# Kernel tuning notes

Hardware: AMD Instinct MI355X
Metric: run time of the kernel (lower is better)

The kernel has to match this reference:

```python
import jax, jax.numpy as jnp
import numpy as np

B, N = 256, 16384


def setup_inputs() -> dict:
    key = jax.random.key(0)
    k1, k2, k3 = jax.random.split(key, 3)
    pred_coords = jax.random.normal(k1, (B, N, 3), dtype=jnp.float32)
    true_coords = jax.random.normal(k2, (B, N, 3), dtype=jnp.float32)
    weights = jax.random.uniform(k3, (B, N), dtype=jnp.float32)
    mask = jnp.ones((B, N), dtype=bool)
    return {"pred_coords": pred_coords, "true_coords": true_coords,
            "weights": weights, "mask": mask}


def reference(pred_coords, true_coords, weights, mask):
    # Mask out invalid atoms (Algorithm 28, weighted Kabsch alignment)
    pred = jnp.where(mask[..., None], pred_coords, 0.0)
    true = jnp.where(mask[..., None], true_coords, 0.0)
    w = jnp.where(mask, weights, 0.0)[..., None]            # [b, n, 1]

    wsum = w.sum(axis=1, keepdims=True)                     # [b, 1, 1]
    pred_centroid = (pred * w).sum(axis=1, keepdims=True) / wsum
    true_centroid = (true * w).sum(axis=1, keepdims=True) / wsum

    pred_c = pred - pred_centroid                           # [b, n, 3]
    true_c = true - true_centroid                           # [b, n, 3]

    # weighted covariance: [b, 3, 3]
    cov = jnp.einsum('bni,bnj->bij', true_c * w, pred_c)

    # torch.svd returns V (not V^T); jnp returns Vh = V^T. rot = U @ V^T = U @ Vh
    U, _, Vh = jnp.linalg.svd(cov)
    rot = jnp.einsum('bij,bjk->bik', U, Vh)

    # reflection fix: flip last column of V (= last row of Vh) where det < 0
    det = jnp.linalg.det(rot)                               # [b]
    flip = jnp.where(det < 0, -1.0, 1.0)                    # [b]
    Vh_fixed = Vh.at[:, -1, :].multiply(flip[:, None])
    rot = jnp.einsum('bij,bjk->bik', U, Vh_fixed)

    aligned = jnp.einsum('bni,bij->bnj', pred_c, rot) + true_centroid
    # original module calls .detach_() on the output
    return jax.lax.stop_gradient(aligned)
```

## Files before the change

kernel.cpp:

```cpp
#include <hip/hip_runtime.h>
#include <stdint.h>
#include <math.h>

constexpr int BATCH  = 256;
constexpr int NATOM  = 16384;
constexpr int TPB    = 256;
constexpr int APT    = 4;
constexpr int NQ     = 16;

constexpr int C1     = 4;
constexpr int ITERS  = 4;
constexpr int ABLK1  = NATOM / C1;

constexpr int C3     = 16;

typedef float f32x4 __attribute__((ext_vector_type(4)));
typedef int   i32x4 __attribute__((ext_vector_type(4)));

__global__ __launch_bounds__(TPB) void wra_partials(
    const float* __restrict__ pred, const float* __restrict__ tru,
    const float* __restrict__ wgt, const int* __restrict__ mask,
    float* __restrict__ partials)
{
    const int blk = blockIdx.x;
    const int b   = blk >> 2;
    const int s   = blk & 3;
    const int tid = threadIdx.x;

    float acc[NQ];
    #pragma unroll
    for (int k = 0; k < NQ; ++k) acc[k] = 0.f;

    #pragma unroll 2
    for (int it = 0; it < ITERS; ++it) {
        const long base = (long)b * NATOM + (long)s * ABLK1
                        + (long)it * (TPB * APT) + (long)tid * APT;

        const f32x4* p4 = reinterpret_cast<const f32x4*>(pred + base * 3);
        const f32x4* t4 = reinterpret_cast<const f32x4*>(tru  + base * 3);
        f32x4 pA = p4[0], pB = p4[1], pC = p4[2];
        f32x4 tA = __builtin_nontemporal_load(t4 + 0);
        f32x4 tB = __builtin_nontemporal_load(t4 + 1);
        f32x4 tC = __builtin_nontemporal_load(t4 + 2);
        f32x4 wv = __builtin_nontemporal_load(
                       reinterpret_cast<const f32x4*>(wgt + base));
        i32x4 mv = *reinterpret_cast<const i32x4*>(mask + base);

        float P[12] = {pA.x,pA.y,pA.z,pA.w, pB.x,pB.y,pB.z,pB.w, pC.x,pC.y,pC.z,pC.w};
        float T[12] = {tA.x,tA.y,tA.z,tA.w, tB.x,tB.y,tB.z,tB.w, tC.x,tC.y,tC.z,tC.w};
        float W[4]  = {mv.x ? wv.x : 0.f, mv.y ? wv.y : 0.f,
                       mv.z ? wv.z : 0.f, mv.w ? wv.w : 0.f};

        #pragma unroll
        for (int k = 0; k < APT; ++k) {
            float w  = W[k];
            float px = P[3*k], py = P[3*k+1], pz = P[3*k+2];
            float tx = T[3*k], ty = T[3*k+1], tz = T[3*k+2];
            float wtx = w * tx, wty = w * ty, wtz = w * tz;
            acc[0]  += w;
            acc[1]  += w * px;  acc[2]  += w * py;  acc[3]  += w * pz;
            acc[4]  += wtx;     acc[5]  += wty;     acc[6]  += wtz;
            acc[7]  += wtx*px;  acc[8]  += wtx*py;  acc[9]  += wtx*pz;
            acc[10] += wty*px;  acc[11] += wty*py;  acc[12] += wty*pz;
            acc[13] += wtz*px;  acc[14] += wtz*py;  acc[15] += wtz*pz;
        }
    }

    #pragma unroll
    for (int off = 32; off > 0; off >>= 1) {
        #pragma unroll
        for (int k = 0; k < NQ; ++k)
            acc[k] += __shfl_down(acc[k], off, 64);
    }
    __shared__ float red[4][NQ];
    const int wave = tid >> 6, lane = tid & 63;
    if (lane == 0) {
        #pragma unroll
        for (int k = 0; k < NQ; ++k) red[wave][k] = acc[k];
    }
    __syncthreads();
    if (tid < NQ)
        partials[blk * NQ + tid] =
            red[0][tid] + red[1][tid] + red[2][tid] + red[3][tid];
}

__device__ inline void jrot(double M[3][3], double V[3][3], int p, int q) {
    double mpq = M[p][q];
    if (fabs(mpq) < 1e-300) return;
    double theta = (M[q][q] - M[p][p]) / (2.0 * mpq);
    double t = copysign(1.0, theta) / (fabs(theta) + sqrt(theta * theta + 1.0));
    double c = 1.0 / sqrt(t * t + 1.0);
    double s = t * c;
    int r = 3 - p - q;
    double mpp = M[p][p], mqq = M[q][q], mrp = M[r][p], mrq = M[r][q];
    M[p][p] = mpp - t * mpq;
    M[q][q] = mqq + t * mpq;
    M[p][q] = M[q][p] = 0.0;
    double nrp = c * mrp - s * mrq;
    double nrq = s * mrp + c * mrq;
    M[r][p] = M[p][r] = nrp;
    M[r][q] = M[q][r] = nrq;
    #pragma unroll
    for (int i = 0; i < 3; ++i) {
        double vip = V[i][p], viq = V[i][q];
        V[i][p] = c * vip - s * viq;
        V[i][q] = s * vip + c * viq;
    }
}

__global__ __launch_bounds__(64) void wra_solve(
    const float* __restrict__ partials, float* __restrict__ consts)
{
    const int b = blockIdx.x, tid = threadIdx.x;
    __shared__ double q[NQ];
    if (tid < NQ) {
        double sum = 0.0;
        for (int s = 0; s < C1; ++s)
            sum += (double)partials[(b * C1 + s) * NQ + tid];
        q[tid] = sum;
    }
    __syncthreads();
    if (tid != 0) return;

    double wsum = q[0];
    double pc[3], tc[3];
    for (int j = 0; j < 3; ++j) { pc[j] = q[1+j] / wsum; tc[j] = q[4+j] / wsum; }

    double C[3][3];
    for (int i = 0; i < 3; ++i)
        for (int j = 0; j < 3; ++j)
            C[i][j] = q[7 + 3*i + j] - wsum * tc[i] * pc[j];

    double M[3][3];
    for (int i = 0; i < 3; ++i)
        for (int j = 0; j < 3; ++j)
            M[i][j] = C[0][i]*C[0][j] + C[1][i]*C[1][j] + C[2][i]*C[2][j];
    double V[3][3] = {{1,0,0},{0,1,0},{0,0,1}};
    for (int sweep = 0; sweep < 12; ++sweep) {
        double off = M[0][1]*M[0][1] + M[0][2]*M[0][2] + M[1][2]*M[1][2];
        double diag = M[0][0] + M[1][1] + M[2][2];
        if (off <= 1e-28 * diag * diag) break;
        jrot(M, V, 0, 1);
        jrot(M, V, 0, 2);
        jrot(M, V, 1, 2);
    }
    double lam[3] = {M[0][0], M[1][1], M[2][2]};
    int i0 = 0, i1 = 1, i2 = 2, tmp;
    if (lam[i0] < lam[i1]) { tmp = i0; i0 = i1; i1 = tmp; }
    if (lam[i0] < lam[i2]) { tmp = i0; i0 = i2; i2 = tmp; }
    if (lam[i1] < lam[i2]) { tmp = i1; i1 = i2; i2 = tmp; }
    double v0[3] = {V[0][i0], V[1][i0], V[2][i0]};
    double v1[3] = {V[0][i1], V[1][i1], V[2][i1]};
    double v2[3] = {V[0][i2], V[1][i2], V[2][i2]};

    double u0[3], u1[3];
    for (int i = 0; i < 3; ++i) {
        u0[i] = C[i][0]*v0[0] + C[i][1]*v0[1] + C[i][2]*v0[2];
        u1[i] = C[i][0]*v1[0] + C[i][1]*v1[1] + C[i][2]*v1[2];
    }
    double n0 = sqrt(u0[0]*u0[0] + u0[1]*u0[1] + u0[2]*u0[2]);
    for (int i = 0; i < 3; ++i) u0[i] /= n0;
    double d01 = u1[0]*u0[0] + u1[1]*u0[1] + u1[2]*u0[2];
    for (int i = 0; i < 3; ++i) u1[i] -= d01 * u0[i];
    double n1 = sqrt(u1[0]*u1[0] + u1[1]*u1[1] + u1[2]*u1[2]);
    for (int i = 0; i < 3; ++i) u1[i] /= n1;

    double detV = v0[0]*(v1[1]*v2[2] - v1[2]*v2[1])
                - v0[1]*(v1[0]*v2[2] - v1[2]*v2[0])
                + v0[2]*(v1[0]*v2[1] - v1[1]*v2[0]);
    double sV = (detV >= 0.0) ? 1.0 : -1.0;
    double u2[3] = { sV * (u0[1]*u1[2] - u0[2]*u1[1]),
                     sV * (u0[2]*u1[0] - u0[0]*u1[2]),
                     sV * (u0[0]*u1[1] - u0[1]*u1[0]) };

    float* out = consts + b * 15;
    for (int i = 0; i < 3; ++i)
        for (int j = 0; j < 3; ++j)
            out[3*i + j] = (float)(u0[i]*v0[j] + u1[i]*v1[j] + u2[i]*v2[j]);
    for (int j = 0; j < 3; ++j) { out[9 + j] = (float)pc[j]; out[12 + j] = (float)tc[j]; }
}

__global__ __launch_bounds__(TPB) void wra_apply(
    const float* __restrict__ pred, const int* __restrict__ mask,
    const float* __restrict__ consts, float* __restrict__ out)
{
    const int blk = blockIdx.x;
    const int b   = blk >> 4;
    const int s   = blk & 15;
    const int tid = threadIdx.x;

    __shared__ float c[15];
    if (tid < 15) c[tid] = consts[b * 15 + tid];
    __syncthreads();

    const long base = (long)b * NATOM + (long)s * (TPB * APT) + (long)tid * APT;
    const f32x4* p4 = reinterpret_cast<const f32x4*>(pred + base * 3);
    f32x4 pA = p4[0], pB = p4[1], pC = p4[2];
    i32x4 mv = *reinterpret_cast<const i32x4*>(mask + base);

    float P[12] = {pA.x,pA.y,pA.z,pA.w, pB.x,pB.y,pB.z,pB.w, pC.x,pC.y,pC.z,pC.w};
    int Mk[4] = {mv.x, mv.y, mv.z, mv.w};
    float O[12];

    #pragma unroll
    for (int k = 0; k < APT; ++k) {
        float px = (Mk[k] ? P[3*k]   : 0.f) - c[9];
        float py = (Mk[k] ? P[3*k+1] : 0.f) - c[10];
        float pz = (Mk[k] ? P[3*k+2] : 0.f) - c[11];
        O[3*k]   = px * c[0] + py * c[3] + pz * c[6] + c[12];
        O[3*k+1] = px * c[1] + py * c[4] + pz * c[7] + c[13];
        O[3*k+2] = px * c[2] + py * c[5] + pz * c[8] + c[14];
    }
    f32x4* o4 = reinterpret_cast<f32x4*>(out + base * 3);
    f32x4 o0 = {O[0], O[1], O[2],  O[3]};
    f32x4 o1 = {O[4], O[5], O[6],  O[7]};
    f32x4 o2 = {O[8], O[9], O[10], O[11]};
    __builtin_nontemporal_store(o0, o4 + 0);
    __builtin_nontemporal_store(o1, o4 + 1);
    __builtin_nontemporal_store(o2, o4 + 2);
}

extern "C" void kernel_launch(void* const* d_in, const int* in_sizes, int n_in,
                              void* d_out, int out_size, void* d_ws, size_t ws_size,
                              hipStream_t stream) {
    const float* pred = (const float*)d_in[0];
    const float* tru  = (const float*)d_in[1];
    const float* wgt  = (const float*)d_in[2];
    const int*   mask = (const int*)d_in[3];
    float* out = (float*)d_out;

    float* partials = (float*)d_ws;
    float* consts   = partials + BATCH * C1 * NQ;

    hipLaunchKernelGGL(wra_partials, dim3(BATCH * C1), dim3(TPB), 0, stream,
                       pred, tru, wgt, mask, partials);
    hipLaunchKernelGGL(wra_solve, dim3(BATCH), dim3(64), 0, stream,
                       partials, consts);
    hipLaunchKernelGGL(wra_apply, dim3(BATCH * C3), dim3(TPB), 0, stream,
                       pred, mask, consts, out);
}
```

Before: 192.8 us.

## Fuse partial reduction, SVD solve and apply into one kernel with flag sync

Merges the three kernels into a single kernel. The last block per batch, detected by an atomic counter, solves the 3x3 alignment, and all four blocks spin-wait on a per-batch flag before applying the rotation to their own atoms. Because each block re-reads the pred chunk it just streamed, that read can hit cache, and two launch boundaries disappear. The cost is an extra memset launch and a cross-block spin-wait: if not all 1024 blocks are co-resident, this relies on scheduling and a bounded timeout, which could produce wrong output if it expires.

```diff
diff --git a/kernel.cpp b/kernel.cpp
--- a/kernel.cpp
+++ b/kernel.cpp
@@ -2,86 +2,40 @@
 #include <stdint.h>
 #include <math.h>
 
-constexpr int BATCH  = 256;
-constexpr int NATOM  = 16384;
-constexpr int TPB    = 256;
-constexpr int APT    = 4;
-constexpr int NQ     = 16;
-
-constexpr int C1     = 4;
-constexpr int ITERS  = 4;
-constexpr int ABLK1  = NATOM / C1;
-
-constexpr int C3     = 16;
+constexpr int BATCH = 256;
+constexpr int NATOM = 16384;
+constexpr int TPB   = 256;
+constexpr int NQ    = 16;
+constexpr int C     = 4;
+constexpr int ABLK  = NATOM / C;
+constexpr int GRAN  = 4;
+
 
 typedef float f32x4 __attribute__((ext_vector_type(4)));
 typedef int   i32x4 __attribute__((ext_vector_type(4)));
 
-__global__ __launch_bounds__(TPB) void wra_partials(
-    const float* __restrict__ pred, const float* __restrict__ tru,
-    const float* __restrict__ wgt, const int* __restrict__ mask,
-    float* __restrict__ partials)
+__device__ __forceinline__ void accum4(
+    const f32x4 p0, const f32x4 p1, const f32x4 p2,
+    const f32x4 t0, const f32x4 t1, const f32x4 t2,
+    const f32x4 wv, const i32x4 mv, float* acc)
 {
-    const int blk = blockIdx.x;
-    const int b   = blk >> 2;
-    const int s   = blk & 3;
-    const int tid = threadIdx.x;
-
-    float acc[NQ];
-    #pragma unroll
-    for (int k = 0; k < NQ; ++k) acc[k] = 0.f;
-
-    #pragma unroll 2
-    for (int it = 0; it < ITERS; ++it) {
-        const long base = (long)b * NATOM + (long)s * ABLK1
-                        + (long)it * (TPB * APT) + (long)tid * APT;
-
-        const f32x4* p4 = reinterpret_cast<const f32x4*>(pred + base * 3);
-        const f32x4* t4 = reinterpret_cast<const f32x4*>(tru  + base * 3);
-        f32x4 pA = p4[0], pB = p4[1], pC = p4[2];
-        f32x4 tA = __builtin_nontemporal_load(t4 + 0);
-        f32x4 tB = __builtin_nontemporal_load(t4 + 1);
-        f32x4 tC = __builtin_nontemporal_load(t4 + 2);
-        f32x4 wv = __builtin_nontemporal_load(
-                       reinterpret_cast<const f32x4*>(wgt + base));
-        i32x4 mv = *reinterpret_cast<const i32x4*>(mask + base);
-
-        float P[12] = {pA.x,pA.y,pA.z,pA.w, pB.x,pB.y,pB.z,pB.w, pC.x,pC.y,pC.z,pC.w};
-        float T[12] = {tA.x,tA.y,tA.z,tA.w, tB.x,tB.y,tB.z,tB.w, tC.x,tC.y,tC.z,tC.w};
-        float W[4]  = {mv.x ? wv.x : 0.f, mv.y ? wv.y : 0.f,
-                       mv.z ? wv.z : 0.f, mv.w ? wv.w : 0.f};
-
-        #pragma unroll
-        for (int k = 0; k < APT; ++k) {
-            float w  = W[k];
-            float px = P[3*k], py = P[3*k+1], pz = P[3*k+2];
-            float tx = T[3*k], ty = T[3*k+1], tz = T[3*k+2];
-            float wtx = w * tx, wty = w * ty, wtz = w * tz;
-            acc[0]  += w;
-            acc[1]  += w * px;  acc[2]  += w * py;  acc[3]  += w * pz;
-            acc[4]  += wtx;     acc[5]  += wty;     acc[6]  += wtz;
-            acc[7]  += wtx*px;  acc[8]  += wtx*py;  acc[9]  += wtx*pz;
-            acc[10] += wty*px;  acc[11] += wty*py;  acc[12] += wty*pz;
-            acc[13] += wtz*px;  acc[14] += wtz*py;  acc[15] += wtz*pz;
-        }
-    }
-
-    #pragma unroll
-    for (int off = 32; off > 0; off >>= 1) {
-        #pragma unroll
-        for (int k = 0; k < NQ; ++k)
-            acc[k] += __shfl_down(acc[k], off, 64);
-    }
-    __shared__ float red[4][NQ];
-    const int wave = tid >> 6, lane = tid & 63;
-    if (lane == 0) {
-        #pragma unroll
-        for (int k = 0; k < NQ; ++k) red[wave][k] = acc[k];
-    }
-    __syncthreads();
-    if (tid < NQ)
-        partials[blk * NQ + tid] =
-            red[0][tid] + red[1][tid] + red[2][tid] + red[3][tid];
+    const float pf[12] = {p0.x,p0.y,p0.z,p0.w, p1.x,p1.y,p1.z,p1.w, p2.x,p2.y,p2.z,p2.w};
+    const float tf[12] = {t0.x,t0.y,t0.z,t0.w, t1.x,t1.y,t1.z,t1.w, t2.x,t2.y,t2.z,t2.w};
+    const float wf[4]  = {wv.x, wv.y, wv.z, wv.w};
+    const int   mf[4]  = {mv.x, mv.y, mv.z, mv.w};
+    #pragma unroll
+    for (int k = 0; k < 4; ++k) {
+        const float w  = (mf[k] != 0) ? wf[k] : 0.f;
+        const float px = pf[3*k], py = pf[3*k+1], pz = pf[3*k+2];
+        const float tx = tf[3*k], ty = tf[3*k+1], tz = tf[3*k+2];
+        const float wtx = w * tx, wty = w * ty, wtz = w * tz;
+        acc[0]  += w;
+        acc[1]  += w * px;  acc[2]  += w * py;  acc[3]  += w * pz;
+        acc[4]  += wtx;     acc[5]  += wty;     acc[6]  += wtz;
+        acc[7]  += wtx*px;  acc[8]  += wtx*py;  acc[9]  += wtx*pz;
+        acc[10] += wty*px;  acc[11] += wty*py;  acc[12] += wty*pz;
+        acc[13] += wtz*px;  acc[14] += wtz*py;  acc[15] += wtz*pz;
+    }
 }
 
 __device__ inline void jrot(double M[3][3], double V[3][3], int p, int q) {
@@ -108,116 +62,193 @@
     }
 }
 
-__global__ __launch_bounds__(64) void wra_solve(
-    const float* __restrict__ partials, float* __restrict__ consts)
-{
-    const int b = blockIdx.x, tid = threadIdx.x;
-    __shared__ double q[NQ];
-    if (tid < NQ) {
-        double sum = 0.0;
-        for (int s = 0; s < C1; ++s)
-            sum += (double)partials[(b * C1 + s) * NQ + tid];
-        q[tid] = sum;
-    }
-    __syncthreads();
-    if (tid != 0) return;
-
-    double wsum = q[0];
-    double pc[3], tc[3];
-    for (int j = 0; j < 3; ++j) { pc[j] = q[1+j] / wsum; tc[j] = q[4+j] / wsum; }
-
-    double C[3][3];
-    for (int i = 0; i < 3; ++i)
-        for (int j = 0; j < 3; ++j)
-            C[i][j] = q[7 + 3*i + j] - wsum * tc[i] * pc[j];
-
-    double M[3][3];
-    for (int i = 0; i < 3; ++i)
-        for (int j = 0; j < 3; ++j)
-            M[i][j] = C[0][i]*C[0][j] + C[1][i]*C[1][j] + C[2][i]*C[2][j];
-    double V[3][3] = {{1,0,0},{0,1,0},{0,0,1}};
-    for (int sweep = 0; sweep < 12; ++sweep) {
-        double off = M[0][1]*M[0][1] + M[0][2]*M[0][2] + M[1][2]*M[1][2];
-        double diag = M[0][0] + M[1][1] + M[2][2];
-        if (off <= 1e-28 * diag * diag) break;
-        jrot(M, V, 0, 1);
-        jrot(M, V, 0, 2);
-        jrot(M, V, 1, 2);
-    }
-    double lam[3] = {M[0][0], M[1][1], M[2][2]};
-    int i0 = 0, i1 = 1, i2 = 2, tmp;
-    if (lam[i0] < lam[i1]) { tmp = i0; i0 = i1; i1 = tmp; }
-    if (lam[i0] < lam[i2]) { tmp = i0; i0 = i2; i2 = tmp; }
-    if (lam[i1] < lam[i2]) { tmp = i1; i1 = i2; i2 = tmp; }
-    double v0[3] = {V[0][i0], V[1][i0], V[2][i0]};
-    double v1[3] = {V[0][i1], V[1][i1], V[2][i1]};
-    double v2[3] = {V[0][i2], V[1][i2], V[2][i2]};
-
-    double u0[3], u1[3];
-    for (int i = 0; i < 3; ++i) {
-        u0[i] = C[i][0]*v0[0] + C[i][1]*v0[1] + C[i][2]*v0[2];
-        u1[i] = C[i][0]*v1[0] + C[i][1]*v1[1] + C[i][2]*v1[2];
-    }
-    double n0 = sqrt(u0[0]*u0[0] + u0[1]*u0[1] + u0[2]*u0[2]);
-    for (int i = 0; i < 3; ++i) u0[i] /= n0;
-    double d01 = u1[0]*u0[0] + u1[1]*u0[1] + u1[2]*u0[2];
-    for (int i = 0; i < 3; ++i) u1[i] -= d01 * u0[i];
-    double n1 = sqrt(u1[0]*u1[0] + u1[1]*u1[1] + u1[2]*u1[2]);
-    for (int i = 0; i < 3; ++i) u1[i] /= n1;
-
-    double detV = v0[0]*(v1[1]*v2[2] - v1[2]*v2[1])
-                - v0[1]*(v1[0]*v2[2] - v1[2]*v2[0])
-                + v0[2]*(v1[0]*v2[1] - v1[1]*v2[0]);
-    double sV = (detV >= 0.0) ? 1.0 : -1.0;
-    double u2[3] = { sV * (u0[1]*u1[2] - u0[2]*u1[1]),
-                     sV * (u0[2]*u1[0] - u0[0]*u1[2]),
-                     sV * (u0[0]*u1[1] - u0[1]*u1[0]) };
-
-    float* out = consts + b * 15;
-    for (int i = 0; i < 3; ++i)
-        for (int j = 0; j < 3; ++j)
-            out[3*i + j] = (float)(u0[i]*v0[j] + u1[i]*v1[j] + u2[i]*v2[j]);
-    for (int j = 0; j < 3; ++j) { out[9 + j] = (float)pc[j]; out[12 + j] = (float)tc[j]; }
-}
-
-__global__ __launch_bounds__(TPB) void wra_apply(
-    const float* __restrict__ pred, const int* __restrict__ mask,
-    const float* __restrict__ consts, float* __restrict__ out)
+#define LOADG(Sfx, g) do {                                                   \
+    const long base_ = base0 + (long)(g) * (TPB * 4);                        \
+    const f32x4* p4_ = reinterpret_cast<const f32x4*>(pred + base_ * 3);     \
+    const f32x4* t4_ = reinterpret_cast<const f32x4*>(tru  + base_ * 3);     \
+    p##Sfx##0 = p4_[0]; p##Sfx##1 = p4_[1]; p##Sfx##2 = p4_[2];              \
+    t##Sfx##0 = t4_[0]; t##Sfx##1 = t4_[1]; t##Sfx##2 = t4_[2];              \
+    w##Sfx = *reinterpret_cast<const f32x4*>(wgt + base_);                   \
+    m##Sfx = *reinterpret_cast<const i32x4*>(mask + base_);                  \
+} while (0)
+
+__global__ __launch_bounds__(TPB, 4) void wra_fused(
+    const float* __restrict__ pred, const float* __restrict__ tru,
+    const float* __restrict__ wgt, const int* __restrict__ mask,
+    int* cnt, int* flag, float* partials, float* consts,
+    float* __restrict__ out)
 {
     const int blk = blockIdx.x;
-    const int b   = blk >> 4;
-    const int s   = blk & 15;
+    const int b   = blk >> 2;
+    const int s   = blk & 3;
     const int tid = threadIdx.x;
-
-    __shared__ float c[15];
-    if (tid < 15) c[tid] = consts[b * 15 + tid];
-    __syncthreads();
-
-    const long base = (long)b * NATOM + (long)s * (TPB * APT) + (long)tid * APT;
-    const f32x4* p4 = reinterpret_cast<const f32x4*>(pred + base * 3);
-    f32x4 pA = p4[0], pB = p4[1], pC = p4[2];
-    i32x4 mv = *reinterpret_cast<const i32x4*>(mask + base);
-
-    float P[12] = {pA.x,pA.y,pA.z,pA.w, pB.x,pB.y,pB.z,pB.w, pC.x,pC.y,pC.z,pC.w};
-    int Mk[4] = {mv.x, mv.y, mv.z, mv.w};
-    float O[12];
-
-    #pragma unroll
-    for (int k = 0; k < APT; ++k) {
-        float px = (Mk[k] ? P[3*k]   : 0.f) - c[9];
-        float py = (Mk[k] ? P[3*k+1] : 0.f) - c[10];
-        float pz = (Mk[k] ? P[3*k+2] : 0.f) - c[11];
-        O[3*k]   = px * c[0] + py * c[3] + pz * c[6] + c[12];
-        O[3*k+1] = px * c[1] + py * c[4] + pz * c[7] + c[13];
-        O[3*k+2] = px * c[2] + py * c[5] + pz * c[8] + c[14];
-    }
-    f32x4* o4 = reinterpret_cast<f32x4*>(out + base * 3);
-    f32x4 o0 = {O[0], O[1], O[2],  O[3]};
-    f32x4 o1 = {O[4], O[5], O[6],  O[7]};
-    f32x4 o2 = {O[8], O[9], O[10], O[11]};
-    __builtin_nontemporal_store(o0, o4 + 0);
-    __builtin_nontemporal_store(o1, o4 + 1);
-    __builtin_nontemporal_store(o2, o4 + 2);
+    const long base0 = (long)b * NATOM + (long)s * ABLK + (long)tid * 4;
+
+    float acc[NQ];
+    #pragma unroll
+    for (int k = 0; k < NQ; ++k) acc[k] = 0.f;
+
+    f32x4 pA0, pA1, pA2, tA0, tA1, tA2, wA;
+    f32x4 pB0, pB1, pB2, tB0, tB1, tB2, wB;
+    i32x4 mA, mB;
+
+    LOADG(A, 0);
+    LOADG(B, 1);
+    accum4(pA0, pA1, pA2, tA0, tA1, tA2, wA, mA, acc);
+    LOADG(A, 2);
+    accum4(pB0, pB1, pB2, tB0, tB1, tB2, wB, mB, acc);
+    LOADG(B, 3);
+    accum4(pA0, pA1, pA2, tA0, tA1, tA2, wA, mA, acc);
+    accum4(pB0, pB1, pB2, tB0, tB1, tB2, wB, mB, acc);
+
+    #pragma unroll
+    for (int off = 32; off >= 4; off >>= 1) {
+        #pragma unroll
+        for (int k = 0; k < NQ; ++k)
+            acc[k] += __shfl_down(acc[k], off, 64);
+    }
+    __shared__ float red[16][NQ + 1];
+    const int wave = tid >> 6, lane = tid & 63;
+    if (lane < 4) {
+        #pragma unroll
+        for (int k = 0; k < NQ; ++k) red[wave * 4 + lane][k] = acc[k];
+    }
+    __syncthreads();
+    if (tid < NQ) {
+        float ssum = 0.f;
+        #pragma unroll
+        for (int r = 0; r < 16; ++r) ssum += red[r][tid];
+        partials[blk * NQ + tid] = ssum;
+    }
+    __threadfence();
+
+    __shared__ int amLast;
+    __syncthreads();
+    if (tid == 0) {
+        int prev = __hip_atomic_fetch_add(&cnt[b], 1, __ATOMIC_ACQ_REL,
+                                          __HIP_MEMORY_SCOPE_AGENT);
+        amLast = (prev == C - 1);
+    }
+    __syncthreads();
+
+    if (amLast) {
+        __shared__ double q[NQ];
+        if (tid < NQ) {
+            double sum = 0.0;
+            for (int cidx = 0; cidx < C; ++cidx)
+                sum += (double)partials[(b * C + cidx) * NQ + tid];
+            q[tid] = sum;
+        }
+        __syncthreads();
+        if (tid == 0) {
+            double wsum = q[0];
+            double pc[3], tc[3];
+            for (int j = 0; j < 3; ++j) { pc[j] = q[1+j] / wsum; tc[j] = q[4+j] / wsum; }
+
+            double Cv[3][3];
+            for (int i = 0; i < 3; ++i)
+                for (int j = 0; j < 3; ++j)
+                    Cv[i][j] = q[7 + 3*i + j] - wsum * tc[i] * pc[j];
+
+            double M[3][3];
+            for (int i = 0; i < 3; ++i)
+                for (int j = 0; j < 3; ++j)
+                    M[i][j] = Cv[0][i]*Cv[0][j] + Cv[1][i]*Cv[1][j] + Cv[2][i]*Cv[2][j];
+            double V[3][3] = {{1,0,0},{0,1,0},{0,0,1}};
+            for (int sweep = 0; sweep < 12; ++sweep) {
+                double off = M[0][1]*M[0][1] + M[0][2]*M[0][2] + M[1][2]*M[1][2];
+                double diag = M[0][0] + M[1][1] + M[2][2];
+                if (off <= 1e-28 * diag * diag) break;
+                jrot(M, V, 0, 1);
+                jrot(M, V, 0, 2);
+                jrot(M, V, 1, 2);
+            }
+            double lam[3] = {M[0][0], M[1][1], M[2][2]};
+            int i0 = 0, i1 = 1, i2 = 2, tmp;
+            if (lam[i0] < lam[i1]) { tmp = i0; i0 = i1; i1 = tmp; }
+            if (lam[i0] < lam[i2]) { tmp = i0; i0 = i2; i2 = tmp; }
+            if (lam[i1] < lam[i2]) { tmp = i1; i1 = i2; i2 = tmp; }
+            double v0[3] = {V[0][i0], V[1][i0], V[2][i0]};
+            double v1[3] = {V[0][i1], V[1][i1], V[2][i1]};
+            double v2[3] = {V[0][i2], V[1][i2], V[2][i2]};
+
+            double u0[3], u1[3];
+            for (int i = 0; i < 3; ++i) {
+                u0[i] = Cv[i][0]*v0[0] + Cv[i][1]*v0[1] + Cv[i][2]*v0[2];
+                u1[i] = Cv[i][0]*v1[0] + Cv[i][1]*v1[1] + Cv[i][2]*v1[2];
+            }
+            double n0 = sqrt(u0[0]*u0[0] + u0[1]*u0[1] + u0[2]*u0[2]);
+            for (int i = 0; i < 3; ++i) u0[i] /= n0;
+            double d01 = u1[0]*u0[0] + u1[1]*u0[1] + u1[2]*u0[2];
+            for (int i = 0; i < 3; ++i) u1[i] -= d01 * u0[i];
+            double n1 = sqrt(u1[0]*u1[0] + u1[1]*u1[1] + u1[2]*u1[2]);
+            for (int i = 0; i < 3; ++i) u1[i] /= n1;
+
+            double detV = v0[0]*(v1[1]*v2[2] - v1[2]*v2[1])
+                        - v0[1]*(v1[0]*v2[2] - v1[2]*v2[0])
+                        + v0[2]*(v1[0]*v2[1] - v1[1]*v2[0]);
+            double sV = (detV >= 0.0) ? 1.0 : -1.0;
+            double u2[3] = { sV * (u0[1]*u1[2] - u0[2]*u1[1]),
+                             sV * (u0[2]*u1[0] - u0[0]*u1[2]),
+                             sV * (u0[0]*u1[1] - u0[1]*u1[0]) };
+
+            float* o = consts + b * 15;
+            for (int i = 0; i < 3; ++i)
+                for (int j = 0; j < 3; ++j)
+                    o[3*i + j] = (float)(u0[i]*v0[j] + u1[i]*v1[j] + u2[i]*v2[j]);
+            for (int j = 0; j < 3; ++j) { o[9 + j] = (float)pc[j]; o[12 + j] = (float)tc[j]; }
+
+            __threadfence();
+            __hip_atomic_store(&flag[b], 1, __ATOMIC_RELEASE,
+                               __HIP_MEMORY_SCOPE_AGENT);
+        }
+    }
+
+    if (tid == 0) {
+        int iter = 0;
+        while (__hip_atomic_load(&flag[b], __ATOMIC_ACQUIRE,
+                                 __HIP_MEMORY_SCOPE_AGENT) == 0) {
+            __builtin_amdgcn_s_sleep(16);
+            if (++iter > (1 << 20)) break;
+        }
+    }
+    __syncthreads();
+
+    __shared__ float cst[15];
+    if (tid < 15) cst[tid] = consts[b * 15 + tid];
+    __syncthreads();
+
+    const float pcx = cst[9],  pcy = cst[10], pcz = cst[11];
+    const float tcx = cst[12], tcy = cst[13], tcz = cst[14];
+
+    #pragma unroll
+    for (int g = 0; g < GRAN; ++g) {
+        const long base = base0 + (long)g * (TPB * 4);
+        const f32x4* p4 = reinterpret_cast<const f32x4*>(pred + base * 3);
+        f32x4 P0 = p4[0], P1 = p4[1], P2 = p4[2];
+        i32x4 mv = *reinterpret_cast<const i32x4*>(mask + base);
+
+        const float pf[12] = {P0.x,P0.y,P0.z,P0.w, P1.x,P1.y,P1.z,P1.w,
+                              P2.x,P2.y,P2.z,P2.w};
+        const int   mf[4]  = {mv.x, mv.y, mv.z, mv.w};
+        float O[12];
+        #pragma unroll
+        for (int k = 0; k < 4; ++k) {
+            const float px = (mf[k] ? pf[3*k]   : 0.f) - pcx;
+            const float py = (mf[k] ? pf[3*k+1] : 0.f) - pcy;
+            const float pz = (mf[k] ? pf[3*k+2] : 0.f) - pcz;
+            O[3*k]     = px * cst[0] + py * cst[3] + pz * cst[6] + tcx;
+            O[3*k + 1] = px * cst[1] + py * cst[4] + pz * cst[7] + tcy;
+            O[3*k + 2] = px * cst[2] + py * cst[5] + pz * cst[8] + tcz;
+        }
+        f32x4* o4 = reinterpret_cast<f32x4*>(out + base * 3);
+        f32x4 o0 = {O[0], O[1], O[2],  O[3]};
+        f32x4 o1 = {O[4], O[5], O[6],  O[7]};
+        f32x4 o2 = {O[8], O[9], O[10], O[11]};
+        __builtin_nontemporal_store(o0, o4 + 0);
+        __builtin_nontemporal_store(o1, o4 + 1);
+        __builtin_nontemporal_store(o2, o4 + 2);
+    }
 }
 
 extern "C" void kernel_launch(void* const* d_in, const int* in_sizes, int n_in,
@@ -229,13 +260,12 @@
     const int*   mask = (const int*)d_in[3];
     float* out = (float*)d_out;
 
-    float* partials = (float*)d_ws;
-    float* consts   = partials + BATCH * C1 * NQ;
-
-    hipLaunchKernelGGL(wra_partials, dim3(BATCH * C1), dim3(TPB), 0, stream,
-                       pred, tru, wgt, mask, partials);
-    hipLaunchKernelGGL(wra_solve, dim3(BATCH), dim3(64), 0, stream,
-                       partials, consts);
-    hipLaunchKernelGGL(wra_apply, dim3(BATCH * C3), dim3(TPB), 0, stream,
-                       pred, mask, consts, out);
-}
+    int*   cnt      = (int*)d_ws;
+    int*   flag     = cnt + BATCH;
+    float* partials = (float*)(flag + BATCH);
+    float* consts   = partials + BATCH * C * NQ;
+
+    hipMemsetAsync(d_ws, 0, 2 * BATCH * sizeof(int), stream);
+    hipLaunchKernelGGL(wra_fused, dim3(BATCH * C), dim3(TPB), 0, stream,
+                       pred, tru, wgt, mask, cnt, flag, partials, consts, out);
+}
```

Result: slower. 500.2 us (+159.5%).
